# Optimization experiments

Hardware: AMD Instinct MI355X
Metric: run time of the kernel (lower is better)

The kernel has to match this reference:

```python
import jax, jax.numpy as jnp
import numpy as np

N, E_RAW, F_IN, H, C = 50000, 800000, 500, 5, 32
HID = H * C  # 160
NEG_GAT = 0.2   # GATConv leaky_relu slope for attention logits
NEG = 0.01      # F.leaky_relu default slope
LN_EPS = 1e-5


def glorot(key, shape):
    fan_in, fan_out = shape[0], shape[-1]
    lim = jnp.sqrt(6.0 / (fan_in + fan_out))
    return jax.random.uniform(key, shape, jnp.float32, -lim, lim)


def setup_inputs() -> dict:
    key = jax.random.key(0)
    ks = jax.random.split(key, 12)
    x = jax.random.normal(ks[0], (N, F_IN), jnp.float32)
    edge_index = jax.random.randint(ks[1], (2, E_RAW), 0, N, jnp.int64)
    return {
        "x": x,
        "edge_index": edge_index,
        "W1": glorot(ks[2], (F_IN, HID)),
        "att1_s": glorot(ks[3], (H, C)),
        "att1_d": glorot(ks[4], (H, C)),
        "b1": jnp.zeros((HID,), jnp.float32),
        "g1": jnp.ones((HID,), jnp.float32),
        "be1": jnp.zeros((HID,), jnp.float32),
        "W2": glorot(ks[5], (HID, HID)),
        "att2_s": glorot(ks[6], (H, C)),
        "att2_d": glorot(ks[7], (H, C)),
        "b2": jnp.zeros((HID,), jnp.float32),
        "Wm": glorot(ks[8], (HID, HID)),
        "bm": jnp.zeros((HID,), jnp.float32),
    }


def add_self_loops(edge_index):
    loops = jnp.arange(N, dtype=edge_index.dtype)
    return jnp.concatenate([edge_index, jnp.stack([loops, loops])], axis=1)


def gat_conv(x, src, dst, W, att_s, att_d, bias):
    # x: [N, Fin] -> per-head transform [N, H, C]
    xl = (x @ W).reshape(N, H, C)
    a_s = jnp.einsum('nhc,hc->nh', xl, att_s)  # [N, H]
    a_d = jnp.einsum('nhc,hc->nh', xl, att_d)
    logits = jax.nn.leaky_relu(a_s[src] + a_d[dst], NEG_GAT)  # [E, H]
    # segment softmax over incoming edges of each dst node
    lmax = jax.ops.segment_max(logits, dst, num_segments=N)
    alpha = jnp.exp(logits - lmax[dst])
    denom = jax.ops.segment_sum(alpha, dst, num_segments=N)
    alpha = alpha / (denom[dst] + 1e-16)
    msg = xl[src] * alpha[:, :, None]  # [E, H, C]
    out = jax.ops.segment_sum(msg, dst, num_segments=N)
    return out.reshape(N, HID) + bias, alpha


def layer_norm(x, g, b):
    mu = jnp.mean(x, axis=-1, keepdims=True)
    var = jnp.mean((x - mu) ** 2, axis=-1, keepdims=True)
    return (x - mu) * jax.lax.rsqrt(var + LN_EPS) * g + b


def reference(x, edge_index, W1, att1_s, att1_d, b1, g1, be1,
              W2, att2_s, att2_d, b2, Wm, bm):
    ei = add_self_loops(edge_index)
    src, dst = ei[0], ei[1]
    h, alpha1 = gat_conv(x, src, dst, W1, att1_s, att1_d, b1)
    h = jax.nn.leaky_relu(h, NEG)
    h = layer_norm(h, g1, be1)  # dropout is identity in eval mode
    h, alpha2 = gat_conv(h, src, dst, W2, att2_s, att2_d, b2)
    h = jax.nn.leaky_relu(h, NEG)
    out = jax.nn.leaky_relu(h @ Wm + bm, NEG)
    return out, alpha1, alpha2
```

## Files before the change

### kernel.cpp

```cpp
#include <hip/hip_runtime.h>

#define N_NODES 50000
#define E_RAW_N 800000
#define E_TOT   850000
#define F_IN_K  500
#define HID     160

using short8 = __attribute__((ext_vector_type(8))) short;
using f32x4  = __attribute__((ext_vector_type(4))) float;

__device__ __forceinline__ float b2f(unsigned short u) {
  union { unsigned int i; float f; } v; v.i = ((unsigned int)u) << 16; return v.f;
}
__device__ __forceinline__ unsigned short f2b(float f) {
  union { float f; unsigned int i; } v; v.f = f;
  unsigned int i = v.i;
  unsigned int lsb = (i >> 16) & 1u;
  i += 0x7fffu + lsb;
  return (unsigned short)(i >> 16);
}

__device__ __forceinline__ float wsum(float x) {
  #pragma unroll
  for (int o = 32; o; o >>= 1) x += __shfl_xor(x, o, 64);
  return x;
}
__device__ __forceinline__ float wmax(float x) {
  #pragma unroll
  for (int o = 32; o; o >>= 1) x = fmaxf(x, __shfl_xor(x, o, 64));
  return x;
}
__device__ __forceinline__ float lrelu2(float x) { return x > 0.f ? x : 0.2f * x; }

__global__ void detect_kernel(const int* __restrict__ ei, int* __restrict__ flag) {
  if (threadIdx.x == 0 && blockIdx.x == 0) {
    int allz = 1;
    for (int i = 1; i < 128; i += 2) if (ei[i] != 0) { allz = 0; break; }
    *flag = allz;
  }
}
__device__ __forceinline__ int edge_src(const int* ei, int wide, int e) {
  return wide ? ei[2 * e] : ei[e];
}
__device__ __forceinline__ int edge_dst(const int* ei, int wide, int e) {
  return wide ? ei[2 * (E_RAW_N + e)] : ei[E_RAW_N + e];
}

__global__ __launch_bounds__(256) void convert_all(
    const float* __restrict__ W1, const float* __restrict__ W2, const float* __restrict__ Wm,
    unsigned short* __restrict__ Bt1, unsigned short* __restrict__ Bt2,
    unsigned short* __restrict__ Btm)
{
  const int i = blockIdx.x * 256 + threadIdx.x;
  if (i < HID * 512) {
    const int c = i / 512, k = i % 512;
    Bt1[i] = f2b((k < F_IN_K) ? W1[(long)k * HID + c] : 0.f);
  }
  if (i < HID * 192) {
    const int c = i / 192, k = i % 192;
    Bt2[i] = f2b((k < HID) ? W2[(long)k * HID + c] : 0.f);
    Btm[i] = f2b((k < HID) ? Wm[(long)k * HID + c] : 0.f);
  }
}

template<typename AT, int K, int KPAD, int BK, int MODE>
__global__ __launch_bounds__(256) void gemm_lds(
    const AT* __restrict__ A, const unsigned short* __restrict__ Bt,
    float* __restrict__ C, unsigned short* __restrict__ Ch,
    const float* __restrict__ bias,
    const float* __restrict__ att_s, const float* __restrict__ att_d,
    float* __restrict__ a_s, float* __restrict__ a_d)
{
  constexpr bool AB16 = (sizeof(AT) == 2);
  constexpr int LSTR = BK + 8;
  constexpr int CHUNKS = KPAD / BK;
  constexpr int KSC = BK / 32;
  constexpr int ROWU = BK / 8;
  constexpr int UNITS = HID * ROWU;
  static_assert(UNITS % 256 == 0, "units must tile threads");
  constexpr int UPT = UNITS / 256;
  __shared__ __align__(16) unsigned short Bs[HID][LSTR];

  const int t = threadIdx.x;
  const int l = t & 63;
  const int w = t >> 6;
  const int m = l & 15;
  const int kgrp = (l >> 4) * 8;
  const int rbase = blockIdx.x * 64 + w * 16;
  const int arow = (rbase + m < N_NODES) ? rbase + m : N_NODES - 1;
  const AT* Arow = A + (long)arow * K;

  f32x4 acc[10];
  #pragma unroll
  for (int i = 0; i < 10; ++i) acc[i] = (f32x4){0.f, 0.f, 0.f, 0.f};

  short8 rb[UPT];
  float  arF[KSC][8], arF2[KSC][8];
  short8 arS[KSC], arS2[KSC];

  auto loadB = [&](int cc, short8* dst) {
    #pragma unroll
    for (int i = 0; i < UPT; ++i) {
      const int u = i * 256 + t;
      const int c = u / ROWU;
      const int k8 = u % ROWU;
      dst[i] = *(const short8*)(Bt + (long)c * KPAD + cc * BK + k8 * 8);
    }
  };
  auto loadA = [&](int cc, float aF[KSC][8], short8* aS) {
    #pragma unroll
    for (int ks = 0; ks < KSC; ++ks) {
      const int kb = cc * BK + ks * 32 + kgrp;
      if constexpr (AB16) {
        short8 v = (short8){0,0,0,0,0,0,0,0};
        if (kb + 8 <= K) v = *(const short8*)(Arow + kb);
        else if (kb < K) {
          #pragma unroll
          for (int j = 0; j < 8; ++j) v[j] = (kb + j < K) ? (short)Arow[kb + j] : (short)0;
        }
        aS[ks] = v;
      } else {
        if (kb + 8 <= K) {
          const float4 a0 = *(const float4*)(Arow + kb);
          const float4 a1 = *(const float4*)(Arow + kb + 4);
          aF[ks][0]=a0.x; aF[ks][1]=a0.y; aF[ks][2]=a0.z; aF[ks][3]=a0.w;
          aF[ks][4]=a1.x; aF[ks][5]=a1.y; aF[ks][6]=a1.z; aF[ks][7]=a1.w;
        } else {
          #pragma unroll
          for (int j = 0; j < 8; ++j) aF[ks][j] = (kb + j < K) ? (float)Arow[kb + j] : 0.f;
        }
      }
    }
  };

  loadB(0, rb);
  loadA(0, arF, arS);

  for (int cc = 0; cc < CHUNKS; ++cc) {
    __syncthreads();
    #pragma unroll
    for (int i = 0; i < UPT; ++i) {
      const int u = i * 256 + t;
      const int c = u / ROWU;
      const int k8 = u % ROWU;
      *(short8*)&Bs[c][k8 * 8] = rb[i];
    }
    __syncthreads();
    if (cc + 1 < CHUNKS) {
      loadB(cc + 1, rb);
      loadA(cc + 1, arF2, arS2);
      __builtin_amdgcn_sched_barrier(0);
    }
    __builtin_amdgcn_s_setprio(1);
    #pragma unroll
    for (int ks = 0; ks < KSC; ++ks) {
      short8 ah;
      if constexpr (AB16) {
        ah = arS[ks];
      } else {
        #pragma unroll
        for (int j = 0; j < 8; ++j) ah[j] = (short)f2b(arF[ks][j]);
      }
      #pragma unroll
      for (int ct = 0; ct < 10; ++ct) {
        const short8 bh = *(const short8*)&Bs[ct * 16 + m][ks * 32 + kgrp];
        acc[ct] = __builtin_amdgcn_mfma_f32_16x16x32_bf16(ah, bh, acc[ct], 0, 0, 0);
      }
    }
    __builtin_amdgcn_s_setprio(0);
    if (cc + 1 < CHUNKS) {
      #pragma unroll
      for (int ks = 0; ks < KSC; ++ks) {
        if constexpr (AB16) arS[ks] = arS2[ks];
        else {
          #pragma unroll
          for (int j = 0; j < 8; ++j) arF[ks][j] = arF2[ks][j];
        }
      }
    }
  }

  const int crow0 = rbase + (l >> 4) * 4;

  if (MODE == 2) {
    #pragma unroll
    for (int r = 0; r < 4; ++r) {
      float ps[5], pd[5];
      #pragma unroll
      for (int h = 0; h < 5; ++h) {
        float s = acc[2*h][r]     * att_s[(2*h) * 16 + m]
                + acc[2*h + 1][r] * att_s[(2*h + 1) * 16 + m];
        float d = acc[2*h][r]     * att_d[(2*h) * 16 + m]
                + acc[2*h + 1][r] * att_d[(2*h + 1) * 16 + m];
        #pragma unroll
        for (int o = 1; o < 16; o <<= 1) {
          s += __shfl_xor(s, o, 64);
          d += __shfl_xor(d, o, 64);
        }
        ps[h] = s; pd[h] = d;
      }
      const int crow = crow0 + r;
      if (crow < N_NODES && m < 5) {
        const float vs = m == 0 ? ps[0] : m == 1 ? ps[1] : m == 2 ? ps[2] : m == 3 ? ps[3] : ps[4];
        const float vd = m == 0 ? pd[0] : m == 1 ? pd[1] : m == 2 ? pd[2] : m == 3 ? pd[3] : pd[4];
        a_s[crow * 5 + m] = vs;
        a_d[crow * 5 + m] = vd;
      }
    }
  }

  #pragma unroll
  for (int r = 0; r < 4; ++r) {
    const int crow = crow0 + r;
    if (crow < N_NODES) {
      #pragma unroll
      for (int ct = 0; ct < 10; ++ct) {
        const int col = ct * 16 + m;
        float v = acc[ct][r];
        if (MODE == 1) { v += bias[col]; v = v > 0.f ? v : 0.01f * v; }
        if (MODE == 2) Ch[(long)crow * HID + col] = f2b(v);
        else           C[(long)crow * HID + col] = v;
      }
    }
  }
}

__global__ __launch_bounds__(256) void count_kernel(const int* __restrict__ ei,
    const int* __restrict__ flag, int* __restrict__ deg) {
  const int e = blockIdx.x * 256 + threadIdx.x;
  if (e >= E_TOT) return;
  const int wide = *flag;
  const int d = (e < E_RAW_N) ? edge_dst(ei, wide, e) : (e - E_RAW_N);
  atomicAdd(&deg[d], 1);
}

#define SCAN_CHUNK 49
__global__ __launch_bounds__(1024) void scan_kernel(const int* __restrict__ deg, int* __restrict__ off) {
  __shared__ int wtot[16];
  const int t = threadIdx.x;
  const int lane = t & 63, wid = t >> 6;
  const int base = t * SCAN_CHUNK;
  int local[SCAN_CHUNK];
  int sum = 0;
  #pragma unroll
  for (int i = 0; i < SCAN_CHUNK; ++i) {
    const int idx = base + i;
    const int v = (idx < N_NODES) ? deg[idx] : 0;
    local[i] = sum;
    sum += v;
  }
  int inc = sum;
  #pragma unroll
  for (int o = 1; o < 64; o <<= 1) {
    const int y = __shfl_up(inc, o, 64);
    if (lane >= o) inc += y;
  }
  if (lane == 63) wtot[wid] = inc;
  __syncthreads();
  if (wid == 0 && lane < 16) {
    const int v = wtot[lane];
    int inc2 = v;
    #pragma unroll
    for (int o = 1; o < 16; o <<= 1) {
      const int y = __shfl_up(inc2, o, 64);
      if (lane >= o) inc2 += y;
    }
    wtot[lane] = inc2 - v;
  }
  __syncthreads();
  const int pre = wtot[wid] + (inc - sum);
  #pragma unroll
  for (int i = 0; i < SCAN_CHUNK; ++i) {
    const int idx = base + i;
    if (idx < N_NODES) off[idx] = pre + local[i];
  }
  if (t == 1023) off[N_NODES] = E_TOT;
}

__global__ __launch_bounds__(256) void fill_kernel(const int* __restrict__ ei,
    const int* __restrict__ flag, const int* __restrict__ off,
    int* __restrict__ fillc, int* __restrict__ csr_src, int* __restrict__ csr_eid) {
  const int e = blockIdx.x * 256 + threadIdx.x;
  if (e >= E_TOT) return;
  const int wide = *flag;
  int s, d;
  if (e < E_RAW_N) { s = edge_src(ei, wide, e); d = edge_dst(ei, wide, e); }
  else { s = e - E_RAW_N; d = s; }
  const int p = off[d] + atomicAdd(&fillc[d], 1);
  csr_src[p] = s;
  csr_eid[p] = e;
}

template<int DO_LN>
__global__ __launch_bounds__(256) void node_kernel(
    const int* __restrict__ off_, const int* __restrict__ csr_src, const int* __restrict__ csr_eid,
    const unsigned short* __restrict__ xlh,
    const float* __restrict__ a_s, const float* __restrict__ a_d,
    float* __restrict__ alpha_out,
    const float* __restrict__ bias,
    const float* __restrict__ gamma_, const float* __restrict__ beta_,
    unsigned short* __restrict__ hout)
{
  __shared__ int   srcS[4][64];
  __shared__ float alS[4][64][6];

  const int w = threadIdx.x >> 6;
  const int l = threadIdx.x & 63;
  const int n = blockIdx.x * 4 + w;
  if (n >= N_NODES) return;
  const int off = off_[n];
  const int deg = off_[n + 1] - off;

  const float ad0 = a_d[n*5+0], ad1 = a_d[n*5+1], ad2 = a_d[n*5+2], ad3 = a_d[n*5+3], ad4 = a_d[n*5+4];
  const int hA = l >> 4;
  float accx = 0.f, accy = 0.f, accz = 0.f;

  if (deg <= 64) {
    int src = 0, eid = 0;
    float v0 = -1e30f, v1 = -1e30f, v2 = -1e30f, v3 = -1e30f, v4 = -1e30f;
    if (l < deg) {
      src = csr_src[off + l];
      eid = csr_eid[off + l];
      const float* ap = a_s + src * 5;
      v0 = lrelu2(ap[0] + ad0);
      v1 = lrelu2(ap[1] + ad1);
      v2 = lrelu2(ap[2] + ad2);
      v3 = lrelu2(ap[3] + ad3);
      v4 = lrelu2(ap[4] + ad4);
    }
    const float m0 = wmax(v0), m1 = wmax(v1), m2 = wmax(v2), m3 = wmax(v3), m4 = wmax(v4);
    float e0 = 0.f, e1 = 0.f, e2 = 0.f, e3 = 0.f, e4 = 0.f;
    if (l < deg) {
      e0 = __expf(v0 - m0); e1 = __expf(v1 - m1); e2 = __expf(v2 - m2);
      e3 = __expf(v3 - m3); e4 = __expf(v4 - m4);
    }
    const float i0 = 1.f / (wsum(e0) + 1e-16f), i1 = 1.f / (wsum(e1) + 1e-16f),
                i2 = 1.f / (wsum(e2) + 1e-16f), i3 = 1.f / (wsum(e3) + 1e-16f),
                i4 = 1.f / (wsum(e4) + 1e-16f);
    const float a0 = e0 * i0, a1 = e1 * i1, a2 = e2 * i2, a3 = e3 * i3, a4 = e4 * i4;
    if (l < deg) {
      float* aw = alpha_out + (long)eid * 5;
      aw[0] = a0; aw[1] = a1; aw[2] = a2; aw[3] = a3; aw[4] = a4;
    }
    srcS[w][l] = src;
    alS[w][l][0] = a0; alS[w][l][1] = a1; alS[w][l][2] = a2;
    alS[w][l][3] = a3; alS[w][l][4] = a4;

    const int degR = (deg + 7) & ~7;
    const unsigned cx = 2 * l, cz = 128 + l;
    for (int s0 = 0; s0 < degR; s0 += 8) {
      int sr[8]; float aA[8], aB[8];
      #pragma unroll
      for (int j = 0; j < 8; ++j) {
        sr[j] = srcS[w][s0 + j];
        aA[j] = alS[w][s0 + j][hA];
        aB[j] = alS[w][s0 + j][4];
      }
      ushort2 u2[8]; unsigned short z[8];
      #pragma unroll
      for (int j = 0; j < 8; ++j) {
        const unsigned xb = (unsigned)sr[j] * HID;
        u2[j] = *(const ushort2*)(xlh + xb + cx);
        if (l < 32) z[j] = xlh[xb + cz];
      }
      #pragma unroll
      for (int j = 0; j < 8; ++j) {
        accx += b2f(u2[j].x) * aA[j];
        accy += b2f(u2[j].y) * aA[j];
        if (l < 32) accz += b2f(z[j]) * aB[j];
      }
    }
  } else {
    float m0 = -1e30f, m1 = -1e30f, m2 = -1e30f, m3 = -1e30f, m4 = -1e30f;
    for (int s = l; s < deg; s += 64) {
      const float* ap = a_s + csr_src[off + s] * 5;
      m0 = fmaxf(m0, lrelu2(ap[0] + ad0));
      m1 = fmaxf(m1, lrelu2(ap[1] + ad1));
      m2 = fmaxf(m2, lrelu2(ap[2] + ad2));
      m3 = fmaxf(m3, lrelu2(ap[3] + ad3));
      m4 = fmaxf(m4, lrelu2(ap[4] + ad4));
    }
    m0 = wmax(m0); m1 = wmax(m1); m2 = wmax(m2); m3 = wmax(m3); m4 = wmax(m4);
    float s0 = 0.f, s1 = 0.f, s2 = 0.f, s3 = 0.f, s4 = 0.f;
    for (int s = l; s < deg; s += 64) {
      const float* ap = a_s + csr_src[off + s] * 5;
      s0 += __expf(lrelu2(ap[0] + ad0) - m0);
      s1 += __expf(lrelu2(ap[1] + ad1) - m1);
      s2 += __expf(lrelu2(ap[2] + ad2) - m2);
      s3 += __expf(lrelu2(ap[3] + ad3) - m3);
      s4 += __expf(lrelu2(ap[4] + ad4) - m4);
    }
    const float i0 = 1.f / (wsum(s0) + 1e-16f), i1 = 1.f / (wsum(s1) + 1e-16f),
                i2 = 1.f / (wsum(s2) + 1e-16f), i3 = 1.f / (wsum(s3) + 1e-16f),
                i4 = 1.f / (wsum(s4) + 1e-16f);
    const float adA = hA == 0 ? ad0 : hA == 1 ? ad1 : hA == 2 ? ad2 : ad3;
    const float mA  = hA == 0 ? m0  : hA == 1 ? m1  : hA == 2 ? m2  : m3;
    const float iA  = hA == 0 ? i0  : hA == 1 ? i1  : hA == 2 ? i2  : i3;
    float adw = 0.f, mw = 0.f, iw = 0.f;
    if (l < 5) {
      adw = l == 0 ? ad0 : l == 1 ? ad1 : l == 2 ? ad2 : l == 3 ? ad3 : ad4;
      mw  = l == 0 ? m0  : l == 1 ? m1  : l == 2 ? m2  : l == 3 ? m3  : m4;
      iw  = l == 0 ? i0  : l == 1 ? i1  : l == 2 ? i2  : l == 3 ? i3  : i4;
    }
    for (int s = 0; s < deg; ++s) {
      const int p = off + s;
      const int srcs = csr_src[p];
      const float* ap = a_s + srcs * 5;
      const float aA = __expf(lrelu2(ap[hA] + adA) - mA) * iA;
      const long xb = (long)srcs * HID;
      const ushort2 u2 = *(const ushort2*)(xlh + xb + 2 * l);
      accx += b2f(u2.x) * aA;
      accy += b2f(u2.y) * aA;
      if (l < 32) {
        const float aC = __expf(lrelu2(ap[4] + ad4) - m4) * i4;
        accz += b2f(xlh[xb + 128 + l]) * aC;
      }
      if (l < 5) {
        alpha_out[(long)csr_eid[p] * 5 + l] = __expf(lrelu2(ap[l] + adw) - mw) * iw;
      }
    }
  }

  const int c0 = 2 * l, c2 = 128 + l;
  float v0 = accx + bias[c0];     v0 = v0 > 0.f ? v0 : 0.01f * v0;
  float v1 = accy + bias[c0 + 1]; v1 = v1 > 0.f ? v1 : 0.01f * v1;
  float v2 = 0.f;
  if (l < 32) { v2 = accz + bias[c2]; v2 = v2 > 0.f ? v2 : 0.01f * v2; }

  const long hb = (long)n * HID;
  if (DO_LN) {
    const float tot = wsum(v0 + v1 + v2);
    const float mean = tot * (1.f / 160.f);
    const float d0 = v0 - mean, d1 = v1 - mean;
    float sq = d0 * d0 + d1 * d1;
    float d2 = 0.f;
    if (l < 32) { d2 = v2 - mean; sq += d2 * d2; }
    const float var = wsum(sq) * (1.f / 160.f);
    const float rstd = rsqrtf(var + 1e-5f);
    hout[hb + c0]     = f2b(d0 * rstd * gamma_[c0]     + beta_[c0]);
    hout[hb + c0 + 1] = f2b(d1 * rstd * gamma_[c0 + 1] + beta_[c0 + 1]);
    if (l < 32) hout[hb + c2] = f2b(d2 * rstd * gamma_[c2] + beta_[c2]);
  } else {
    hout[hb + c0]     = f2b(v0);
    hout[hb + c0 + 1] = f2b(v1);
    if (l < 32) hout[hb + c2] = f2b(v2);
  }
}

extern "C" void kernel_launch(void* const* d_in, const int* in_sizes, int n_in,
                              void* d_out, int out_size, void* d_ws, size_t ws_size,
                              hipStream_t stream)
{
  const float* x     = (const float*)d_in[0];
  const int*   ei    = (const int*)d_in[1];
  const float* W1    = (const float*)d_in[2];
  const float* att1s = (const float*)d_in[3];
  const float* att1d = (const float*)d_in[4];
  const float* b1    = (const float*)d_in[5];
  const float* g1    = (const float*)d_in[6];
  const float* be1   = (const float*)d_in[7];
  const float* W2    = (const float*)d_in[8];
  const float* att2s = (const float*)d_in[9];
  const float* att2d = (const float*)d_in[10];
  const float* b2    = (const float*)d_in[11];
  const float* Wm    = (const float*)d_in[12];
  const float* bm    = (const float*)d_in[13];

  float* out    = (float*)d_out;
  float* alpha1 = out + (long)N_NODES * HID;
  float* alpha2 = alpha1 + (long)E_TOT * 5;

  char* p = (char*)d_ws;
  auto alloc = [&](size_t bytes) { void* r = (void*)p; p += (bytes + 255) & ~(size_t)255; return r; };
  unsigned short* hb16 = (unsigned short*)alloc((size_t)N_NODES * HID * 2);
  unsigned short* xlh  = (unsigned short*)alloc((size_t)N_NODES * HID * 2);
  float* as_  = (float*)alloc((size_t)N_NODES * 5 * 4);
  float* ad_  = (float*)alloc((size_t)N_NODES * 5 * 4);
  int* deg    = (int*)alloc((size_t)N_NODES * 4);
  int* fillc  = (int*)alloc((size_t)N_NODES * 4);
  int* off    = (int*)alloc((size_t)(N_NODES + 1) * 4);
  int* csrS   = (int*)alloc((size_t)E_TOT * 4);
  int* csrE   = (int*)alloc((size_t)E_TOT * 4);
  int* flag   = (int*)alloc(256);
  unsigned short* Bt1 = (unsigned short*)alloc((size_t)HID * 512 * 2);
  unsigned short* Bt2 = (unsigned short*)alloc((size_t)HID * 192 * 2);
  unsigned short* Btm = (unsigned short*)alloc((size_t)HID * 192 * 2);

  hipMemsetAsync(deg, 0, (size_t)N_NODES * 4, stream);
  hipMemsetAsync(fillc, 0, (size_t)N_NODES * 4, stream);

  detect_kernel<<<1, 64, 0, stream>>>(ei, flag);
  const int EB = (E_TOT + 255) / 256;
  count_kernel<<<EB, 256, 0, stream>>>(ei, flag, deg);
  scan_kernel<<<1, 1024, 0, stream>>>(deg, off);
  fill_kernel<<<EB, 256, 0, stream>>>(ei, flag, off, fillc, csrS, csrE);

  convert_all<<<(HID * 512 + 255) / 256, 256, 0, stream>>>(W1, W2, Wm, Bt1, Bt2, Btm);

  const int GB = (N_NODES + 63) / 64;

  gemm_lds<float, F_IN_K, 512, 64, 2><<<GB, 256, 0, stream>>>(x, Bt1, nullptr, xlh, nullptr, att1s, att1d, as_, ad_);
  node_kernel<1><<<N_NODES / 4, 256, 0, stream>>>(off, csrS, csrE, xlh, as_, ad_, alpha1, b1, g1, be1, hb16);

  gemm_lds<unsigned short, HID, 192, 64, 2><<<GB, 256, 0, stream>>>(hb16, Bt2, nullptr, xlh, nullptr, att2s, att2d, as_, ad_);
  node_kernel<0><<<N_NODES / 4, 256, 0, stream>>>(off, csrS, csrE, xlh, as_, ad_, alpha2, b2, nullptr, nullptr, hb16);

  gemm_lds<unsigned short, HID, 192, 64, 1><<<GB, 256, 0, stream>>>(hb16, Btm, out, nullptr, bm, nullptr, nullptr, nullptr, nullptr);
}
```

Measured before the change: 404.7 us.

## Interleave source attention scores into padded feature rows and halve GEMM block

Stores the per-node source attention scores as floats inside each bf16 feature row, using a padded row stride, so the edge gather fetches scores and features from the same row. Drops the separate a_s buffer, and removes the max-subtraction pass in the low-degree softmax path. GEMM blocks now cover 32 rows with 128 threads, giving more blocks. Risks include exp overflow without max subtraction, and more B-tile reloads per row in the GEMM.

Measured after the change: 398.8 us. No clear change (-1.4%).

```diff
diff --git a/kernel.cpp b/kernel.cpp
--- a/kernel.cpp
+++ b/kernel.cpp
@@ -5,6 +5,7 @@
 #define E_TOT   850000
 #define F_IN_K  500
 #define HID     160
+#define XSTR    184
 
 using short8 = __attribute__((ext_vector_type(8))) short;
 using f32x4  = __attribute__((ext_vector_type(4))) float;
@@ -64,12 +65,12 @@
 }
 
 template<typename AT, int K, int KPAD, int BK, int MODE>
-__global__ __launch_bounds__(256) void gemm_lds(
+__global__ __launch_bounds__(128) void gemm_lds(
     const AT* __restrict__ A, const unsigned short* __restrict__ Bt,
     float* __restrict__ C, unsigned short* __restrict__ Ch,
     const float* __restrict__ bias,
     const float* __restrict__ att_s, const float* __restrict__ att_d,
-    float* __restrict__ a_s, float* __restrict__ a_d)
+    float* __restrict__ a_d)
 {
   constexpr bool AB16 = (sizeof(AT) == 2);
   constexpr int LSTR = BK + 8;
@@ -77,8 +78,8 @@
   constexpr int KSC = BK / 32;
   constexpr int ROWU = BK / 8;
   constexpr int UNITS = HID * ROWU;
-  static_assert(UNITS % 256 == 0, "units must tile threads");
-  constexpr int UPT = UNITS / 256;
+  static_assert(UNITS % 128 == 0, "units must tile threads");
+  constexpr int UPT = UNITS / 128;
   __shared__ __align__(16) unsigned short Bs[HID][LSTR];
 
   const int t = threadIdx.x;
@@ -86,7 +87,7 @@
   const int w = t >> 6;
   const int m = l & 15;
   const int kgrp = (l >> 4) * 8;
-  const int rbase = blockIdx.x * 64 + w * 16;
+  const int rbase = blockIdx.x * 32 + w * 16;
   const int arow = (rbase + m < N_NODES) ? rbase + m : N_NODES - 1;
   const AT* Arow = A + (long)arow * K;
 
@@ -101,7 +102,7 @@
   auto loadB = [&](int cc, short8* dst) {
     #pragma unroll
     for (int i = 0; i < UPT; ++i) {
-      const int u = i * 256 + t;
+      const int u = i * 128 + t;
       const int c = u / ROWU;
       const int k8 = u % ROWU;
       dst[i] = *(const short8*)(Bt + (long)c * KPAD + cc * BK + k8 * 8);
@@ -140,7 +141,7 @@
     __syncthreads();
     #pragma unroll
     for (int i = 0; i < UPT; ++i) {
-      const int u = i * 256 + t;
+      const int u = i * 128 + t;
       const int c = u / ROWU;
       const int k8 = u % ROWU;
       *(short8*)&Bs[c][k8 * 8] = rb[i];
@@ -203,7 +204,7 @@
       if (crow < N_NODES && m < 5) {
         const float vs = m == 0 ? ps[0] : m == 1 ? ps[1] : m == 2 ? ps[2] : m == 3 ? ps[3] : ps[4];
         const float vd = m == 0 ? pd[0] : m == 1 ? pd[1] : m == 2 ? pd[2] : m == 3 ? pd[3] : pd[4];
-        a_s[crow * 5 + m] = vs;
+        ((float*)(Ch + (long)crow * XSTR + 160))[m] = vs;
         a_d[crow * 5 + m] = vd;
       }
     }
@@ -218,7 +219,7 @@
         const int col = ct * 16 + m;
         float v = acc[ct][r];
         if (MODE == 1) { v += bias[col]; v = v > 0.f ? v : 0.01f * v; }
-        if (MODE == 2) Ch[(long)crow * HID + col] = f2b(v);
+        if (MODE == 2) Ch[(long)crow * XSTR + col] = f2b(v);
         else           C[(long)crow * HID + col] = v;
       }
     }
@@ -295,7 +296,7 @@
 __global__ __launch_bounds__(256) void node_kernel(
     const int* __restrict__ off_, const int* __restrict__ csr_src, const int* __restrict__ csr_eid,
     const unsigned short* __restrict__ xlh,
-    const float* __restrict__ a_s, const float* __restrict__ a_d,
+    const float* __restrict__ a_d,
     float* __restrict__ alpha_out,
     const float* __restrict__ bias,
     const float* __restrict__ gamma_, const float* __restrict__ beta_,
@@ -317,22 +318,16 @@
 
   if (deg <= 64) {
     int src = 0, eid = 0;
-    float v0 = -1e30f, v1 = -1e30f, v2 = -1e30f, v3 = -1e30f, v4 = -1e30f;
+    float e0 = 0.f, e1 = 0.f, e2 = 0.f, e3 = 0.f, e4 = 0.f;
     if (l < deg) {
       src = csr_src[off + l];
       eid = csr_eid[off + l];
-      const float* ap = a_s + src * 5;
-      v0 = lrelu2(ap[0] + ad0);
-      v1 = lrelu2(ap[1] + ad1);
-      v2 = lrelu2(ap[2] + ad2);
-      v3 = lrelu2(ap[3] + ad3);
-      v4 = lrelu2(ap[4] + ad4);
-    }
-    const float m0 = wmax(v0), m1 = wmax(v1), m2 = wmax(v2), m3 = wmax(v3), m4 = wmax(v4);
-    float e0 = 0.f, e1 = 0.f, e2 = 0.f, e3 = 0.f, e4 = 0.f;
-    if (l < deg) {
-      e0 = __expf(v0 - m0); e1 = __expf(v1 - m1); e2 = __expf(v2 - m2);
-      e3 = __expf(v3 - m3); e4 = __expf(v4 - m4);
+      const float* ap = (const float*)(xlh + (unsigned)src * XSTR + 160);
+      e0 = __expf(lrelu2(ap[0] + ad0));
+      e1 = __expf(lrelu2(ap[1] + ad1));
+      e2 = __expf(lrelu2(ap[2] + ad2));
+      e3 = __expf(lrelu2(ap[3] + ad3));
+      e4 = __expf(lrelu2(ap[4] + ad4));
     }
     const float i0 = 1.f / (wsum(e0) + 1e-16f), i1 = 1.f / (wsum(e1) + 1e-16f),
                 i2 = 1.f / (wsum(e2) + 1e-16f), i3 = 1.f / (wsum(e3) + 1e-16f),
@@ -359,7 +354,7 @@
       ushort2 u2[8]; unsigned short z[8];
       #pragma unroll
       for (int j = 0; j < 8; ++j) {
-        const unsigned xb = (unsigned)sr[j] * HID;
+        const unsigned xb = (unsigned)sr[j] * XSTR;
         u2[j] = *(const ushort2*)(xlh + xb + cx);
         if (l < 32) z[j] = xlh[xb + cz];
       }
@@ -373,7 +368,7 @@
   } else {
     float m0 = -1e30f, m1 = -1e30f, m2 = -1e30f, m3 = -1e30f, m4 = -1e30f;
     for (int s = l; s < deg; s += 64) {
-      const float* ap = a_s + csr_src[off + s] * 5;
+      const float* ap = (const float*)(xlh + (unsigned)csr_src[off + s] * XSTR + 160);
       m0 = fmaxf(m0, lrelu2(ap[0] + ad0));
       m1 = fmaxf(m1, lrelu2(ap[1] + ad1));
       m2 = fmaxf(m2, lrelu2(ap[2] + ad2));
@@ -383,7 +378,7 @@
     m0 = wmax(m0); m1 = wmax(m1); m2 = wmax(m2); m3 = wmax(m3); m4 = wmax(m4);
     float s0 = 0.f, s1 = 0.f, s2 = 0.f, s3 = 0.f, s4 = 0.f;
     for (int s = l; s < deg; s += 64) {
-      const float* ap = a_s + csr_src[off + s] * 5;
+      const float* ap = (const float*)(xlh + (unsigned)csr_src[off + s] * XSTR + 160);
       s0 += __expf(lrelu2(ap[0] + ad0) - m0);
       s1 += __expf(lrelu2(ap[1] + ad1) - m1);
       s2 += __expf(lrelu2(ap[2] + ad2) - m2);
@@ -405,9 +400,9 @@
     for (int s = 0; s < deg; ++s) {
       const int p = off + s;
       const int srcs = csr_src[p];
-      const float* ap = a_s + srcs * 5;
+      const unsigned xb = (unsigned)srcs * XSTR;
+      const float* ap = (const float*)(xlh + xb + 160);
       const float aA = __expf(lrelu2(ap[hA] + adA) - mA) * iA;
-      const long xb = (long)srcs * HID;
       const ushort2 u2 = *(const ushort2*)(xlh + xb + 2 * l);
       accx += b2f(u2.x) * aA;
       accy += b2f(u2.y) * aA;
@@ -473,8 +468,7 @@
   char* p = (char*)d_ws;
   auto alloc = [&](size_t bytes) { void* r = (void*)p; p += (bytes + 255) & ~(size_t)255; return r; };
   unsigned short* hb16 = (unsigned short*)alloc((size_t)N_NODES * HID * 2);
-  unsigned short* xlh  = (unsigned short*)alloc((size_t)N_NODES * HID * 2);
-  float* as_  = (float*)alloc((size_t)N_NODES * 5 * 4);
+  unsigned short* xlh  = (unsigned short*)alloc((size_t)N_NODES * XSTR * 2);
   float* ad_  = (float*)alloc((size_t)N_NODES * 5 * 4);
   int* deg    = (int*)alloc((size_t)N_NODES * 4);
   int* fillc  = (int*)alloc((size_t)N_NODES * 4);
@@ -497,13 +491,13 @@
 
   convert_all<<<(HID * 512 + 255) / 256, 256, 0, stream>>>(W1, W2, Wm, Bt1, Bt2, Btm);
 
-  const int GB = (N_NODES + 63) / 64;
-
-  gemm_lds<float, F_IN_K, 512, 64, 2><<<GB, 256, 0, stream>>>(x, Bt1, nullptr, xlh, nullptr, att1s, att1d, as_, ad_);
-  node_kernel<1><<<N_NODES / 4, 256, 0, stream>>>(off, csrS, csrE, xlh, as_, ad_, alpha1, b1, g1, be1, hb16);
-
-  gemm_lds<unsigned short, HID, 192, 64, 2><<<GB, 256, 0, stream>>>(hb16, Bt2, nullptr, xlh, nullptr, att2s, att2d, as_, ad_);
-  node_kernel<0><<<N_NODES / 4, 256, 0, stream>>>(off, csrS, csrE, xlh, as_, ad_, alpha2, b2, nullptr, nullptr, hb16);
-
-  gemm_lds<unsigned short, HID, 192, 64, 1><<<GB, 256, 0, stream>>>(hb16, Btm, out, nullptr, bm, nullptr, nullptr, nullptr, nullptr);
-}
+  const int GB = (N_NODES + 31) / 32;
+
+  gemm_lds<float, F_IN_K, 512, 64, 2><<<GB, 128, 0, stream>>>(x, Bt1, nullptr, xlh, nullptr, att1s, att1d, ad_);
+  node_kernel<1><<<N_NODES / 4, 256, 0, stream>>>(off, csrS, csrE, xlh, ad_, alpha1, b1, g1, be1, hb16);
+
+  gemm_lds<unsigned short, HID, 192, 64, 2><<<GB, 128, 0, stream>>>(hb16, Bt2, nullptr, xlh, nullptr, att2s, att2d, ad_);
+  node_kernel<0><<<N_NODES / 4, 256, 0, stream>>>(off, csrS, csrE, xlh, ad_, alpha2, b2, nullptr, nullptr, hb16);
+
+  gemm_lds<unsigned short, HID, 192, 64, 1><<<GB, 128, 0, stream>>>(hb16, Btm, out, nullptr, bm, nullptr, nullptr, nullptr);
+}
```
